# Optimization experiments

Measured on AMD Instinct MI355X. Metric: run time of the kernel, lower is better.

The kernel has to match this reference:

```python
import jax, jax.numpy as jnp
import numpy as np

H, Wd, Z = 480, 480, 2
BN_EPS = 1e-3  # PointPillars-style BatchNorm1d(eps=1e-3)


def setup_inputs() -> dict:
    key = jax.random.key(0)
    ks = jax.random.split(key, 5)
    bs, seq, N, Cin, C = 2, 1, 20000, 4, 64
    features = jax.random.normal(ks[0], (bs, seq, N, Cin), dtype=jnp.float32)
    cx = jax.random.randint(ks[1], (bs, seq, N), 0, H)
    cy = jax.random.randint(ks[2], (bs, seq, N), 0, Wd)
    cz = jax.random.randint(ks[3], (bs, seq, N), 0, Z)
    coords = jnp.stack([cx, cy, cz], axis=-1).astype(jnp.int64)
    W = jax.random.normal(ks[4], (C, Cin), dtype=jnp.float32) * 0.1
    gamma = jnp.ones((C,), jnp.float32)
    beta = jnp.zeros((C,), jnp.float32)
    running_mean = jnp.zeros((C,), jnp.float32)
    running_var = jnp.ones((C,), jnp.float32)
    return {"features": features, "coords": coords, "W": W, "gamma": gamma,
            "beta": beta, "running_mean": running_mean, "running_var": running_var}


def reference(features, coords, W, gamma, beta, running_mean, running_var):
    bs, seq, N, Cin = features.shape
    feats = features.reshape(bs * seq, N, Cin)          # [B, N, 4]
    co = coords.reshape(bs * seq, N, 3)
    # flattened voxel index: x*W*Z + y*Z + z, in [0, H*W*Z)
    idx = co[:, :, 0] * (Wd * Z) + co[:, :, 1] * Z + co[:, :, 2]  # [B, N]
    # linear (no bias) + BatchNorm1d (inference stats) + ReLU
    x = jnp.einsum('bnc,uc->bnu', feats, W)             # [B, N, 64]
    x = (x - running_mean) * (gamma / jnp.sqrt(running_var + BN_EPS)) + beta
    x = jax.nn.relu(x)
    B, n, c = x.shape
    # scatter-max into a zero-initialized dense grid (matches torch scatter reduce='max' into zeros)
    x_max = jnp.zeros((B, H * Wd * Z, c), x.dtype)
    x_max = x_max.at[jnp.arange(B)[:, None], idx].max(x)  # [B, HWZ, C]
    # [B, HWZ, C] -> [B, C, H, W, Z] -> [B, Z, C, H, W] -> [B, Z*C, H, W]
    x_max = jnp.transpose(x_max, (0, 2, 1)).reshape(B, c, H, Wd, Z)
    x_max = jnp.transpose(x_max, (0, 4, 1, 2, 3)).reshape(B, Z * c, H, Wd)
    x_perm = jnp.transpose(x, (0, 2, 1))                # [B, C, N]
    return x_perm, jnp.squeeze(x_max)
```

## Files before the change

kernel.cpp:

```cpp
#include <hip/hip_runtime.h>

#define HH  480
#define WW  480
#define ZZ  2
#define CC  64
#define CIN 4
#define BN_EPS 1e-3f
#define CTILE 16

__global__ __launch_bounds__(256) void pfn_clear_head(int4* __restrict__ head4)
{
    int i = blockIdx.x * blockDim.x + threadIdx.x;
    head4[i] = make_int4(-1, -1, -1, -1);
}

__global__ __launch_bounds__(256) void pfn_pass_a(
    const float* __restrict__ feats,
    const int*   __restrict__ coords,
    const float* __restrict__ W,
    const float* __restrict__ gamma,
    const float* __restrict__ beta,
    const float* __restrict__ rmean,
    const float* __restrict__ rvar,
    float* __restrict__ out0,
    int*   __restrict__ head,
    int*   __restrict__ nxt,
    int N, int B)
{
    int gid = blockIdx.x * blockDim.x + threadIdx.x;
    int total = B * N;
    if (gid >= total) return;
    int n = gid % N;
    int b = gid / N;

    float4 f = *reinterpret_cast<const float4*>(feats + (long)gid * CIN);

    #pragma unroll 8
    for (int c = 0; c < CC; ++c) {
        float scale = gamma[c] * rsqrtf(rvar[c] + BN_EPS);
        float bias  = beta[c] - rmean[c] * scale;
        float v = f.x * W[c*4+0] + f.y * W[c*4+1] + f.z * W[c*4+2] + f.w * W[c*4+3];
        v = fmaxf(v * scale + bias, 0.0f);
        out0[((long)(b * CC + c)) * N + n] = v;
    }

    int cx = coords[(long)gid*3 + 0];
    int cy = coords[(long)gid*3 + 1];
    int cz = coords[(long)gid*3 + 2];
    int vox = ((b * ZZ + cz) * HH + cx) * WW + cy;
    nxt[gid] = atomicExch(&head[vox], gid);
}

__global__ __launch_bounds__(256) void pfn_pass_b(
    const float* __restrict__ feats,
    const float* __restrict__ W,
    const float* __restrict__ gamma,
    const float* __restrict__ beta,
    const float* __restrict__ rmean,
    const float* __restrict__ rvar,
    const int*   __restrict__ head,
    const int*   __restrict__ nxt,
    float* __restrict__ out1,
    int N, int B)
{
    int bid = blockIdx.x;
    const int ntile = CC / CTILE;
    int ct  = bid % ntile;
    int rem = bid / ntile;
    int h   = rem % HH;
    int z   = (rem / HH) % ZZ;
    int b   = rem / (HH * ZZ);
    const int c0 = ct * CTILE;

    __shared__ float tile[CTILE][WW];
    float4* t4 = reinterpret_cast<float4*>(&tile[0][0]);
    const int n4 = CTILE * WW / 4;

    for (int i = threadIdx.x; i < n4; i += 256)
        t4[i] = make_float4(0.f, 0.f, 0.f, 0.f);
    __syncthreads();

    float scale[CTILE], bias[CTILE], w0[CTILE], w1[CTILE], w2[CTILE], w3[CTILE];
    #pragma unroll
    for (int j = 0; j < CTILE; ++j) {
        int c = c0 + j;
        scale[j] = gamma[c] * rsqrtf(rvar[c] + BN_EPS);
        bias[j]  = beta[c] - rmean[c] * scale[j];
        w0[j] = W[c*4+0]; w1[j] = W[c*4+1]; w2[j] = W[c*4+2]; w3[j] = W[c*4+3];
    }

    const int row_base = ((b * ZZ + z) * HH + h) * WW;
    for (int w = threadIdx.x; w < WW; w += 256) {
        int p = head[row_base + w];
        while (p >= 0) {
            float4 f = *reinterpret_cast<const float4*>(feats + (long)p * CIN);
            #pragma unroll
            for (int j = 0; j < CTILE; ++j) {
                float v = f.x * w0[j] + f.y * w1[j] + f.z * w2[j] + f.w * w3[j];
                v = fmaxf(v * scale[j] + bias[j], 0.0f);
                tile[j][w] = fmaxf(tile[j][w], v);
            }
            p = nxt[p];
        }
    }
    __syncthreads();

    const long plane = (long)HH * WW;
    const long base  = (((long)(b * ZZ + z)) * CC + c0) * plane + (long)h * WW;
    const int w4row = WW / 4;
    for (int i = threadIdx.x; i < n4; i += 256) {
        int c  = i / w4row;
        int w4 = i % w4row;
        *reinterpret_cast<float4*>(out1 + base + (long)c * plane + (long)w4 * 4) = t4[i];
    }
}

__global__ __launch_bounds__(256) void pfn_fallback(
    const float* __restrict__ feats, const int* __restrict__ coords,
    const float* __restrict__ W, const float* __restrict__ gamma,
    const float* __restrict__ beta, const float* __restrict__ rmean,
    const float* __restrict__ rvar, float* __restrict__ out0,
    float* __restrict__ out1, int N, int B)
{
    long gid = (long)blockIdx.x * blockDim.x + threadIdx.x;
    long total = (long)CC * B * N;
    if (gid >= total) return;
    int n = (int)(gid % N); int rem = (int)(gid / N);
    int b = rem % B; int c = rem / B;
    long pt = (long)b * N + n;
    float4 f = *reinterpret_cast<const float4*>(feats + pt * CIN);
    float scale = gamma[c] * rsqrtf(rvar[c] + BN_EPS);
    float bias  = beta[c] - rmean[c] * scale;
    float val = f.x*W[c*4] + f.y*W[c*4+1] + f.z*W[c*4+2] + f.w*W[c*4+3];
    val = fmaxf(val * scale + bias, 0.0f);
    out0[((long)(b * CC + c)) * N + n] = val;
    int cx = coords[pt*3+0], cy = coords[pt*3+1], cz = coords[pt*3+2];
    long o1 = ((((long)(b * ZZ + cz)) * CC + c) * HH + cx) * WW + cy;
    atomicMax(reinterpret_cast<unsigned int*>(out1) + o1, __float_as_uint(val));
}

extern "C" void kernel_launch(void* const* d_in, const int* in_sizes, int n_in,
                              void* d_out, int out_size, void* d_ws, size_t ws_size,
                              hipStream_t stream) {
    const float* feats  = (const float*)d_in[0];
    const int*   coords = (const int*)d_in[1];
    const float* W      = (const float*)d_in[2];
    const float* gamma  = (const float*)d_in[3];
    const float* beta   = (const float*)d_in[4];
    const float* rmean  = (const float*)d_in[5];
    const float* rvar   = (const float*)d_in[6];

    const int B = 2;
    const int N = in_sizes[0] / (B * CIN);

    float* out0 = (float*)d_out;
    long   out0_sz = (long)B * CC * N;
    float* out1 = out0 + out0_sz;

    const size_t head_elems = (size_t)B * ZZ * HH * WW;
    const size_t head_bytes = head_elems * sizeof(int);
    const size_t next_bytes = (size_t)B * N * sizeof(int);

    if (ws_size >= head_bytes + next_bytes) {
        int* head = (int*)d_ws;
        int* nxt  = (int*)((char*)d_ws + head_bytes);

        pfn_clear_head<<<(int)(head_elems / 4 / 256), 256, 0, stream>>>((int4*)head);

        int totalA = B * N;
        pfn_pass_a<<<(totalA + 255) / 256, 256, 0, stream>>>(
            feats, coords, W, gamma, beta, rmean, rvar, out0, head, nxt, N, B);

        int blocksB = B * ZZ * HH * (CC / CTILE);
        pfn_pass_b<<<blocksB, 256, 0, stream>>>(
            feats, W, gamma, beta, rmean, rvar, head, nxt, out1, N, B);
    } else {
        size_t out1_bytes = (size_t)B * ZZ * CC * HH * WW * sizeof(float);
        (void)hipMemsetAsync(out1, 0, out1_bytes, stream);
        long total = (long)CC * B * N;
        pfn_fallback<<<(int)((total + 255) / 256), 256, 0, stream>>>(
            feats, coords, W, gamma, beta, rmean, rvar, out0, out1, N, B);
    }
}
```

Baseline: 61.74 us.

## Replace per-voxel linked lists with per-row bucketed point arrays and LDS atomicMax

```diff
diff --git a/kernel.cpp b/kernel.cpp
--- a/kernel.cpp
+++ b/kernel.cpp
@@ -6,12 +6,15 @@
 #define CC  64
 #define CIN 4
 #define BN_EPS 1e-3f
-#define CTILE 16
+#define ROWS  (2 * ZZ * HH)
+#define MAXR  256
+#define CHALF 32
+#define TPAD  484
 
-__global__ __launch_bounds__(256) void pfn_clear_head(int4* __restrict__ head4)
+__global__ __launch_bounds__(256) void pfn_clear_cnt(int* __restrict__ rowcnt)
 {
     int i = blockIdx.x * blockDim.x + threadIdx.x;
-    head4[i] = make_int4(-1, -1, -1, -1);
+    if (i < ROWS) rowcnt[i] = 0;
 }
 
 __global__ __launch_bounds__(256) void pfn_pass_a(
@@ -22,9 +25,10 @@
     const float* __restrict__ beta,
     const float* __restrict__ rmean,
     const float* __restrict__ rvar,
-    float* __restrict__ out0,
-    int*   __restrict__ head,
-    int*   __restrict__ nxt,
+    float*  __restrict__ out0,
+    float4* __restrict__ rowf4,
+    int*    __restrict__ roww,
+    int*    __restrict__ rowcnt,
     int N, int B)
 {
     int gid = blockIdx.x * blockDim.x + threadIdx.x;
@@ -47,71 +51,74 @@
     int cx = coords[(long)gid*3 + 0];
     int cy = coords[(long)gid*3 + 1];
     int cz = coords[(long)gid*3 + 2];
-    int vox = ((b * ZZ + cz) * HH + cx) * WW + cy;
-    nxt[gid] = atomicExch(&head[vox], gid);
+    int row = (b * ZZ + cz) * HH + cx;
+    int k = atomicAdd(&rowcnt[row], 1);
+    if (k < MAXR) {
+        rowf4[(long)row * MAXR + k] = f;
+        roww [(long)row * MAXR + k] = cy;
+    }
 }
 
-__global__ __launch_bounds__(256) void pfn_pass_b(
-    const float* __restrict__ feats,
-    const float* __restrict__ W,
-    const float* __restrict__ gamma,
-    const float* __restrict__ beta,
-    const float* __restrict__ rmean,
-    const float* __restrict__ rvar,
-    const int*   __restrict__ head,
-    const int*   __restrict__ nxt,
-    float* __restrict__ out1,
-    int N, int B)
+__global__ __launch_bounds__(512) void pfn_pass_b(
+    const float4* __restrict__ rowf4,
+    const int*    __restrict__ roww,
+    const int*    __restrict__ rowcnt,
+    const float*  __restrict__ W,
+    const float*  __restrict__ gamma,
+    const float*  __restrict__ beta,
+    const float*  __restrict__ rmean,
+    const float*  __restrict__ rvar,
+    float* __restrict__ out1)
 {
-    int bid = blockIdx.x;
-    const int ntile = CC / CTILE;
-    int ct  = bid % ntile;
-    int rem = bid / ntile;
-    int h   = rem % HH;
-    int z   = (rem / HH) % ZZ;
-    int b   = rem / (HH * ZZ);
-    const int c0 = ct * CTILE;
+    int bid  = blockIdx.x;
+    int half = bid & 1;
+    int row  = bid >> 1;
+    int h = row % HH;
+    int z = (row / HH) % ZZ;
+    int b = row / (HH * ZZ);
+    const int c0 = half * CHALF;
+    const int tid = threadIdx.x;
 
-    __shared__ float tile[CTILE][WW];
+    __shared__ float tile[CHALF][TPAD];
+    __shared__ float lw[4][CHALF], lsc[CHALF], lbi[CHALF];
+
     float4* t4 = reinterpret_cast<float4*>(&tile[0][0]);
-    const int n4 = CTILE * WW / 4;
-
-    for (int i = threadIdx.x; i < n4; i += 256)
+    const int n4z = CHALF * TPAD / 4;
+    for (int i = tid; i < n4z; i += 512)
         t4[i] = make_float4(0.f, 0.f, 0.f, 0.f);
+    if (tid < CHALF) {
+        int c = c0 + tid;
+        float s = gamma[c] * rsqrtf(rvar[c] + BN_EPS);
+        lsc[tid] = s;
+        lbi[tid] = beta[c] - rmean[c] * s;
+        lw[0][tid] = W[c*4+0]; lw[1][tid] = W[c*4+1];
+        lw[2][tid] = W[c*4+2]; lw[3][tid] = W[c*4+3];
+    }
     __syncthreads();
 
-    float scale[CTILE], bias[CTILE], w0[CTILE], w1[CTILE], w2[CTILE], w3[CTILE];
-    #pragma unroll
-    for (int j = 0; j < CTILE; ++j) {
-        int c = c0 + j;
-        scale[j] = gamma[c] * rsqrtf(rvar[c] + BN_EPS);
-        bias[j]  = beta[c] - rmean[c] * scale[j];
-        w0[j] = W[c*4+0]; w1[j] = W[c*4+1]; w2[j] = W[c*4+2]; w3[j] = W[c*4+3];
-    }
+    int cnt = rowcnt[row];
+    cnt = cnt < MAXR ? cnt : MAXR;
+    const long rb = (long)row * MAXR;
 
-    const int row_base = ((b * ZZ + z) * HH + h) * WW;
-    for (int w = threadIdx.x; w < WW; w += 256) {
-        int p = head[row_base + w];
-        while (p >= 0) {
-            float4 f = *reinterpret_cast<const float4*>(feats + (long)p * CIN);
-            #pragma unroll
-            for (int j = 0; j < CTILE; ++j) {
-                float v = f.x * w0[j] + f.y * w1[j] + f.z * w2[j] + f.w * w3[j];
-                v = fmaxf(v * scale[j] + bias[j], 0.0f);
-                tile[j][w] = fmaxf(tile[j][w], v);
-            }
-            p = nxt[p];
-        }
+    for (int i = tid; i < cnt * CHALF; i += 512) {
+        int j  = i >> 5;
+        int cc = i & (CHALF - 1);
+        float4 f = rowf4[rb + j];
+        int    w = roww [rb + j];
+        float v = f.x*lw[0][cc] + f.y*lw[1][cc] + f.z*lw[2][cc] + f.w*lw[3][cc];
+        v = fmaxf(v * lsc[cc] + lbi[cc], 0.0f);
+        atomicMax(reinterpret_cast<unsigned int*>(&tile[cc][w]), __float_as_uint(v));
     }
     __syncthreads();
 
     const long plane = (long)HH * WW;
-    const long base  = (((long)(b * ZZ + z)) * CC + c0) * plane + (long)h * WW;
+    const long base  = (((long)((b * ZZ + z) * CC + c0)) * HH + h) * WW;
     const int w4row = WW / 4;
-    for (int i = threadIdx.x; i < n4; i += 256) {
+    for (int i = tid; i < CHALF * w4row; i += 512) {
         int c  = i / w4row;
         int w4 = i % w4row;
-        *reinterpret_cast<float4*>(out1 + base + (long)c * plane + (long)w4 * 4) = t4[i];
+        *reinterpret_cast<float4*>(out1 + base + (long)c * plane + (long)w4 * 4)
+            = *reinterpret_cast<const float4*>(&tile[c][w4 * 4]);
     }
 }
 
@@ -157,23 +164,26 @@
     long   out0_sz = (long)B * CC * N;
     float* out1 = out0 + out0_sz;
 
-    const size_t head_elems = (size_t)B * ZZ * HH * WW;
-    const size_t head_bytes = head_elems * sizeof(int);
-    const size_t next_bytes = (size_t)B * N * sizeof(int);
+    const size_t rowf4_bytes = (size_t)ROWS * MAXR * sizeof(float4);
+    const size_t roww_bytes  = (size_t)ROWS * MAXR * sizeof(int);
+    const size_t cnt_bytes   = (size_t)ROWS * sizeof(int);
+    const size_t need = rowf4_bytes + roww_bytes + cnt_bytes;
 
-    if (ws_size >= head_bytes + next_bytes) {
-        int* head = (int*)d_ws;
-        int* nxt  = (int*)((char*)d_ws + head_bytes);
+    if (ws_size >= need) {
+        float4* rowf4  = (float4*)d_ws;
+        int*    roww   = (int*)((char*)d_ws + rowf4_bytes);
+        int*    rowcnt = (int*)((char*)d_ws + rowf4_bytes + roww_bytes);
 
-        pfn_clear_head<<<(int)(head_elems / 4 / 256), 256, 0, stream>>>((int4*)head);
+        pfn_clear_cnt<<<(ROWS + 255) / 256, 256, 0, stream>>>(rowcnt);
 
         int totalA = B * N;
         pfn_pass_a<<<(totalA + 255) / 256, 256, 0, stream>>>(
-            feats, coords, W, gamma, beta, rmean, rvar, out0, head, nxt, N, B);
+            feats, coords, W, gamma, beta, rmean, rvar, out0,
+            rowf4, roww, rowcnt, N, B);
 
-        int blocksB = B * ZZ * HH * (CC / CTILE);
-        pfn_pass_b<<<blocksB, 256, 0, stream>>>(
-            feats, W, gamma, beta, rmean, rvar, head, nxt, out1, N, B);
+        int blocksB = ROWS * (CC / CHALF);
+        pfn_pass_b<<<blocksB, 512, 0, stream>>>(
+            rowf4, roww, rowcnt, W, gamma, beta, rmean, rvar, out1);
     } else {
         size_t out1_bytes = (size_t)B * ZZ * CC * HH * WW * sizeof(float);
         (void)hipMemsetAsync(out1, 0, out1_bytes, stream);
```

New measurement: 55.29 us. 1.12x faster.
